# Optimization experiments

Hardware: AMD Instinct MI355X
Metric: run time of the kernel (lower is better)

Reference implementation:

```python
import jax, jax.numpy as jnp
import numpy as np
import math

H = 512      # d_model
N = 64       # d_state
B = 16
L = 4096
DT_MIN, DT_MAX = 0.001, 0.1


def setup_inputs() -> dict:
    key = jax.random.key(0)
    ks = jax.random.split(key, 6)
    u = jax.random.normal(ks[0], (B, H, L), dtype=jnp.float32)
    # S4DKernel parameters
    C = jax.random.normal(ks[1], (H, N // 2, 2), dtype=jnp.float32)  # view_as_real of cfloat C
    log_dt = (jax.random.uniform(ks[2], (H,), dtype=jnp.float32)
              * (math.log(DT_MAX) - math.log(DT_MIN)) + math.log(DT_MIN))
    log_A_real = jnp.log(0.5 * jnp.ones((H, N // 2), dtype=jnp.float32))
    A_imag = math.pi * jnp.broadcast_to(jnp.arange(N // 2, dtype=jnp.float32), (H, N // 2))
    # S4D parameters
    D = jax.random.normal(ks[3], (H,), dtype=jnp.float32)
    # output_linear: Conv1d(H, 2H, kernel_size=1) -> weight (2H, H), bias (2H,)
    W = jax.random.normal(ks[4], (2 * H, H), dtype=jnp.float32) * (1.0 / math.sqrt(H))
    b = jax.random.normal(ks[5], (2 * H,), dtype=jnp.float32) * 0.01
    return {"u": u, "C": C, "log_dt": log_dt, "log_A_real": log_A_real,
            "A_imag": A_imag, "D": D, "W": W, "b": b}


def _s4d_kernel(C, log_dt, log_A_real, A_imag, L):
    """Generate the (H, L) convolution kernel from diagonal SSM parameters."""
    dt = jnp.exp(log_dt)                                    # (H,)
    Cc = C[..., 0] + 1j * C[..., 1]                         # (H, N/2) complex
    A = -jnp.exp(log_A_real) + 1j * A_imag                  # (H, N/2)
    dtA = A * dt[:, None]                                   # (H, N/2)
    # Vandermonde: exp(dtA * l) for l in [0, L)
    K = jnp.exp(dtA[:, :, None] * jnp.arange(L, dtype=jnp.float32))  # (H, N/2, L)
    Cw = Cc * (jnp.exp(dtA) - 1.0) / A                      # (H, N/2)
    k = 2.0 * jnp.einsum('hn,hnl->hl', Cw, K).real          # (H, L)
    return k


def reference(u, C, log_dt, log_A_real, A_imag, D, W, b):
    Lc = u.shape[-1]
    k = _s4d_kernel(C, log_dt, log_A_real, A_imag, Lc)      # (H, L)
    # FFT long convolution (linear conv via zero-padding to 2L)
    k_f = jnp.fft.rfft(k, n=2 * Lc)                          # (H, L+1)
    u_f = jnp.fft.rfft(u, n=2 * Lc)                          # (B, H, L+1)
    y = jnp.fft.irfft(u_f * k_f, n=2 * Lc)[..., :Lc]         # (B, H, L)
    y = y + u * D[:, None]
    y = jax.nn.gelu(y, approximate=False)                    # torch nn.GELU default
    # output_linear: 1x1 Conv1d (H -> 2H) then GLU over channel dim
    z = jnp.einsum('oh,bhl->bol', W, y) + b[None, :, None]   # (B, 2H, L)
    a, g = jnp.split(z, 2, axis=1)
    return a * jax.nn.sigmoid(g)                             # (B, H, L)
```

## Files before the change

### kernel.cpp

```cpp
#include <hip/hip_runtime.h>

#define BB 16
#define HH 512
#define NH 32
#define LL 4096
#define TCH 64
#define NCH 64
#define KA 128

static_assert(TCH * NCH == LL, "chunking");

typedef __attribute__((ext_vector_type(8))) short bf16x8;
typedef __attribute__((ext_vector_type(4))) float f32x4;

static __device__ __forceinline__ unsigned short f2bf(float x) {
    return __builtin_bit_cast(unsigned short, (__bf16)x);
}
static __device__ __forceinline__ float bf2f(unsigned short b) {
    return __builtin_bit_cast(float, ((unsigned)b) << 16);
}
static __device__ __forceinline__ unsigned pack2(float a, float b) {
    return (unsigned)f2bf(a) | ((unsigned)f2bf(b) << 16);
}
static __device__ __forceinline__ float gelu1(float x) {
    float a = fmaf(0.071354816f * x, x * x, 1.5957691f * x);
    return x * __builtin_amdgcn_rcpf(1.0f + __expf(-a));
}
static __device__ __forceinline__ unsigned gelu_pk(unsigned p) {
    float a = gelu1(bf2f((unsigned short)(p & 0xffffu)));
    float b = gelu1(bf2f((unsigned short)(p >> 16)));
    return pack2(a, b);
}

static __device__ __forceinline__ void gload_lds16(const void* g, void* l) {
#if __has_builtin(__builtin_amdgcn_global_load_lds)
    __builtin_amdgcn_global_load_lds(
        (const __attribute__((address_space(1))) unsigned int*)g,
        (__attribute__((address_space(3))) unsigned int*)l, 16, 0, 0);
#else
    *(uint4*)l = *(const uint4*)g;
#endif
}

__global__ void k0_params(const float* __restrict__ C,
                          const float* __restrict__ log_dt,
                          const float* __restrict__ lAr,
                          const float* __restrict__ Aim,
                          float* __restrict__ c2R,  float* __restrict__ c2I,
                          float* __restrict__ ltR,  float* __restrict__ ltI,
                          float* __restrict__ xrA,  float* __restrict__ xiA)
{
    int tid = blockIdx.x * 256 + threadIdx.x;
    if (tid >= HH * NH) return;
    int h = tid >> 5;
    float dt = expf(log_dt[h]);
    float Ar = -expf(lAr[tid]);
    float Ai = Aim[tid];
    float xr = Ar * dt, xi = Ai * dt;
    xrA[tid] = xr; xiA[tid] = xi;
    float er = expf(xr);
    float lr = er * cosf(xi);
    float li = er * sinf(xi);
    float wr = lr - 1.0f, wi = li;
    float inv = 1.0f / (Ar * Ar + Ai * Ai);
    float qr = (wr * Ar + wi * Ai) * inv;
    float qi = (wi * Ar - wr * Ai) * inv;
    float cr = C[2 * tid], ci = C[2 * tid + 1];
    c2R[tid] =  2.0f * (cr * qr - ci * qi);
    c2I[tid] = -2.0f * (cr * qi + ci * qr);
    float eT = expf((float)TCH * xr);
    float aT = (float)TCH * xi;
    ltR[tid] = eT * cosf(aT);
    ltI[tid] = eT * sinf(aT);
}

__global__ void kw_pack(const float* __restrict__ W, const float* __restrict__ bias,
                        unsigned short* __restrict__ Wp, float* __restrict__ bp)
{
    int tid = blockIdx.x * 256 + threadIdx.x;
    int drow = tid >> 6;
    int kc = (tid & 63) * 8;
    int src = (drow & 1) ? (drow >> 1) + HH : (drow >> 1);
    const float4* s = (const float4*)(W + (size_t)src * HH + kc);
    float4 a = s[0], b4 = s[1];
    uint4 pack;
    pack.x = pack2(a.x, a.y);
    pack.y = pack2(a.z, a.w);
    pack.z = pack2(b4.x, b4.y);
    pack.w = pack2(b4.z, b4.w);
    *(uint4*)(Wp + (size_t)drow * HH + kc) = pack;
    if (tid < 2 * HH)
        bp[tid] = bias[(tid & 1) ? (tid >> 1) + HH : (tid >> 1)];
}

__global__ __launch_bounds__(64) void kA_build(
    const float* __restrict__ c2R, const float* __restrict__ c2I,
    const float* __restrict__ xrA, const float* __restrict__ xiA,
    const float* __restrict__ Dv,
    unsigned short* __restrict__ Apan, unsigned short* __restrict__ Vpan)
{
    int h = blockIdx.x;
    int t = threadIdx.x;
    __shared__ float s_xr[NH], s_xi[NH], s_cr[NH], s_ci[NH], s_k[TCH];
    if (t < NH) {
        s_xr[t] = xrA[h * NH + t]; s_xi[t] = xiA[h * NH + t];
        s_cr[t] = c2R[h * NH + t]; s_ci[t] = c2I[h * NH + t];
    }
    __syncthreads();
    {
        float d = (float)t;
        float acc = 0.f;
#pragma unroll
        for (int n = 0; n < NH; ++n) {
            float er = __expf(s_xr[n] * d);
            float sv, cv; __sincosf(s_xi[n] * d, &sv, &cv);
            acc = fmaf(s_cr[n], er * cv, fmaf(s_ci[n], er * sv, acc));
        }
        s_k[t] = acc;
    }
    __syncthreads();
    float k0d = s_k[0] + Dv[h];
    unsigned short row[KA];
#pragma unroll
    for (int tau = 0; tau < TCH; ++tau)
        row[tau] = f2bf((tau < t) ? s_k[t - tau] : (tau == t ? k0d : 0.f));
    float tp = (float)(t + 1);
#pragma unroll
    for (int n = 0; n < NH; ++n) {
        float er = __expf(s_xr[n] * tp);
        float sv, cv; __sincosf(s_xi[n] * tp, &sv, &cv);
        float pr = er * cv, pi = er * sv;
        row[TCH + 2 * n]     = f2bf(fmaf(s_cr[n], pr,  s_ci[n] * pi));
        row[TCH + 2 * n + 1] = f2bf(fmaf(s_ci[n], pr, -s_cr[n] * pi));
    }
    {
        uint4* dst = (uint4*)(Apan + ((size_t)h * TCH + t) * KA);
        const uint4* src = (const uint4*)row;
#pragma unroll
        for (int i = 0; i < 16; ++i) dst[i] = src[i];
    }
    {
        int n = t >> 1, cm = t & 1;
        float xr = s_xr[n], xi = s_xi[n];
        unsigned short vrow[TCH];
#pragma unroll
        for (int tau = 0; tau < TCH; ++tau) {
            float p = (float)(TCH - 1 - tau);
            float er = __expf(xr * p);
            float sv, cv; __sincosf(xi * p, &sv, &cv);
            vrow[tau] = f2bf(cm ? er * sv : er * cv);
        }
        uint4* vd = (uint4*)(Vpan + ((size_t)h * TCH + t) * TCH);
        const uint4* vs = (const uint4*)vrow;
#pragma unroll
        for (int i = 0; i < 8; ++i) vd[i] = vs[i];
    }
}

__global__ __launch_bounds__(256)
__attribute__((amdgpu_waves_per_eu(4, 4)))
void kBCD(
    const float* __restrict__ u,
    const unsigned short* __restrict__ Apan, const unsigned short* __restrict__ Vpan,
    const float* __restrict__ ltR, const float* __restrict__ ltI,
    unsigned short* __restrict__ yb)
{
    __shared__ unsigned short Sl[4][TCH * TCH];
    int h = blockIdx.x & (HH - 1), g = blockIdx.x >> 9;
    int tid = threadIdx.x;
    int lane = tid & 63, w = tid >> 6;
    int b = g * 4 + w;
    int lrow = lane & 15, hi = lane >> 4, lk8 = hi * 8;
    const float* ug = u + ((size_t)b * HH + h) * LL;
    const unsigned short* Ap = Apan + (size_t)h * TCH * KA;
    const unsigned short* Vp = Vpan + (size_t)h * TCH * TCH;
    char* Sw = (char*)Sl[w];

    bf16x8 ub[2][4];
#pragma unroll
    for (int ks = 0; ks < 2; ++ks)
#pragma unroll
        for (int n = 0; n < 4; ++n) {
            int c = n * 16 + lrow;
            const float* up = ug + c * TCH + ks * 32 + lk8;
            float4 f0 = *(const float4*)up, f1 = *(const float4*)(up + 4);
            bf16x8 v;
            v[0]=f2bf(f0.x); v[1]=f2bf(f0.y); v[2]=f2bf(f0.z); v[3]=f2bf(f0.w);
            v[4]=f2bf(f1.x); v[5]=f2bf(f1.y); v[6]=f2bf(f1.z); v[7]=f2bf(f1.w);
            ub[ks][n] = v;
        }

#pragma unroll
    for (int m = 0; m < 4; ++m) {
        f32x4 accE[4];
#pragma unroll
        for (int n = 0; n < 4; ++n) { f32x4 z = {0.f,0.f,0.f,0.f}; accE[n] = z; }
#pragma unroll
        for (int ks = 0; ks < 2; ++ks) {
            bf16x8 vf = *(const bf16x8*)(Vp + (m * 16 + lrow) * TCH + ks * 32 + lk8);
#pragma unroll
            for (int n = 0; n < 4; ++n)
                accE[n] = __builtin_amdgcn_mfma_f32_16x16x32_bf16(vf, ub[ks][n], accE[n], 0, 0, 0);
        }
        int j0 = m * 16 + hi * 4;
#pragma unroll
        for (int n = 0; n < 4; ++n) {
            int c = n * 16 + lrow;
            uint2 p; p.x = pack2(accE[n][0], accE[n][1]); p.y = pack2(accE[n][2], accE[n][3]);
            *(uint2*)(Sw + c * 128 + ((2 * j0) ^ ((c & 7) << 4))) = p;
        }
    }
    asm volatile("s_waitcnt lgkmcnt(0)" ::: "memory");

    if (lane < NH) {
        int n = lane;
        float ar = ltR[h * NH + n], ai = ltI[h * NH + n];
        float sr = 0.f, si = 0.f;
#pragma unroll
        for (int gg = 0; gg < 8; ++gg) {
            unsigned ev[8];
#pragma unroll
            for (int k = 0; k < 8; ++k)
                ev[k] = *(const unsigned*)(Sw + (gg * 8 + k) * 128 + ((4 * n) ^ (k << 4)));
#pragma unroll
            for (int k = 0; k < 8; ++k) {
                *(unsigned*)(Sw + (gg * 8 + k) * 128 + ((4 * n) ^ (k << 4))) = pack2(sr, si);
                float er = bf2f((unsigned short)(ev[k] & 0xffffu));
                float ei = bf2f((unsigned short)(ev[k] >> 16));
                float nsr = fmaf(ar, sr, fmaf(-ai, si, er));
                float nsi = fmaf(ar, si, fmaf(ai, sr, ei));
                sr = nsr; si = nsi;
            }
        }
    }
    asm volatile("s_waitcnt lgkmcnt(0)" ::: "memory");

    unsigned short* yrow = yb + ((size_t)b * HH + h) * LL;
#pragma unroll
    for (int m = 0; m < 4; ++m) {
        f32x4 acc[4];
#pragma unroll
        for (int n = 0; n < 4; ++n) { f32x4 z = {0.f,0.f,0.f,0.f}; acc[n] = z; }
#pragma unroll
        for (int ks = 0; ks < 2; ++ks) {
            bf16x8 af = *(const bf16x8*)(Ap + (m * 16 + lrow) * KA + ks * 32 + lk8);
#pragma unroll
            for (int n = 0; n < 4; ++n)
                acc[n] = __builtin_amdgcn_mfma_f32_16x16x32_bf16(af, ub[ks][n], acc[n], 0, 0, 0);
        }
#pragma unroll
        for (int ks = 0; ks < 2; ++ks) {
            bf16x8 af = *(const bf16x8*)(Ap + (m * 16 + lrow) * KA + 64 + ks * 32 + lk8);
#pragma unroll
            for (int n = 0; n < 4; ++n) {
                int c = n * 16 + lrow;
                bf16x8 bfr = *(const bf16x8*)(Sw + c * 128 + ((ks * 64 + lk8 * 2) ^ ((c & 7) << 4)));
                acc[n] = __builtin_amdgcn_mfma_f32_16x16x32_bf16(af, bfr, acc[n], 0, 0, 0);
            }
        }
        int t0 = m * 16 + hi * 4;
#pragma unroll
        for (int n = 0; n < 4; ++n) {
            int c = n * 16 + lrow;
            f32x4 v = acc[n];
            uint2 pw;
            pw.x = pack2(v[0], v[1]);
            pw.y = pack2(v[2], v[3]);
            *(uint2*)(yrow + c * TCH + t0) = pw;
        }
    }
}

__global__ __launch_bounds__(256) void kT_transpose(
    const unsigned short* __restrict__ yb, unsigned short* __restrict__ yt)
{
    __shared__ unsigned short T[64][130];
    int bid = blockIdx.x;
    int lt = bid & 31;
    int ht = (bid >> 5) & 7;
    int b  = bid >> 8;
    int t = threadIdx.x;
#pragma unroll
    for (int r = 0; r < 4; ++r) {
        int chunk = r * 256 + t;
        int row = chunk >> 4;
        int c16 = chunk & 15;
        uint4 v = *(const uint4*)(yb + ((size_t)(b * HH + ht * 64 + row)) * LL
                                     + lt * 128 + c16 * 8);
        v.x = gelu_pk(v.x); v.y = gelu_pk(v.y);
        v.z = gelu_pk(v.z); v.w = gelu_pk(v.w);
        *(uint4*)&T[row][c16 * 8] = v;
    }
    __syncthreads();
    int oct = t & 7, lgrp = t >> 3;
    size_t obase = ((size_t)b * LL + (size_t)lt * 128) * HH + ht * 64 + oct * 8;
#pragma unroll
    for (int r = 0; r < 2; ++r) {
        int l = (r * 32 + lgrp) * 2;
        unsigned v[8];
#pragma unroll
        for (int k = 0; k < 8; ++k)
            v[k] = *(const unsigned*)&T[oct * 8 + k][l];
        uint4 w0, w1;
        w0.x = (v[0] & 0xffffu) | (v[1] << 16);
        w0.y = (v[2] & 0xffffu) | (v[3] << 16);
        w0.z = (v[4] & 0xffffu) | (v[5] << 16);
        w0.w = (v[6] & 0xffffu) | (v[7] << 16);
        w1.x = (v[0] >> 16) | (v[1] & 0xffff0000u);
        w1.y = (v[2] >> 16) | (v[3] & 0xffff0000u);
        w1.z = (v[4] >> 16) | (v[5] & 0xffff0000u);
        w1.w = (v[6] >> 16) | (v[7] & 0xffff0000u);
        *(uint4*)(yt + obase + (size_t)l * HH) = w0;
        *(uint4*)(yt + obase + (size_t)(l + 1) * HH) = w1;
    }
}

#define BM 128
#define BN 128
#define BKK 32

__global__ __launch_bounds__(256, 4) void k4_gemm(
    const unsigned short* __restrict__ Wp, const float* __restrict__ bp,
    const unsigned short* __restrict__ yt, float* __restrict__ out)
{
    __shared__ unsigned short As[BM * BKK];
    __shared__ unsigned short Bs[BN * BKK];
    int tid  = threadIdx.x;
    int bidx = (blockIdx.x & 7) * 512 + (blockIdx.x >> 3);
    int mtile = bidx & 7, ntile = bidx >> 3;
    int mbase = mtile * BM, nbase = ntile * BN;
    int lane = tid & 63;
    int wv = tid >> 6;
    int wr = wv >> 1, wc = wv & 1;
    int lrow = lane & 15;
    int hi = lane >> 4;

    f32x4 acc[4][4];
#pragma unroll
    for (int m = 0; m < 4; ++m)
#pragma unroll
        for (int n = 0; n < 4; ++n) { f32x4 z = {0.f,0.f,0.f,0.f}; acc[m][n] = z; }

    for (int kk = 0; kk < HH; kk += BKK) {
#pragma unroll
        for (int p = 0; p < 2; ++p) {
            int chunk = p * 256 + tid;
            int row = chunk >> 2;
            int c16 = chunk & 3;
            int kc  = (c16 ^ ((row >> 1) & 3)) * 8;
            gload_lds16(Wp + (size_t)(mbase + row) * HH + kk + kc, &As[chunk * 8]);
            gload_lds16(yt + (size_t)(nbase + row) * HH + kk + kc, &Bs[chunk * 8]);
        }
        __syncthreads();
        bf16x8 af[4], bfr[4];
#pragma unroll
        for (int m = 0; m < 4; ++m) {
            int row = wr * 64 + m * 16 + lrow;
            int slot = hi ^ ((row >> 1) & 3);
            af[m] = *(const bf16x8*)&As[row * BKK + slot * 8];
        }
#pragma unroll
        for (int nf = 0; nf < 4; ++nf) {
            int row = wc * 64 + nf * 16 + lrow;
            int slot = hi ^ ((row >> 1) & 3);
            bfr[nf] = *(const bf16x8*)&Bs[row * BKK + slot * 8];
        }
#pragma unroll
        for (int m = 0; m < 4; ++m)
#pragma unroll
            for (int nf = 0; nf < 4; ++nf)
                acc[m][nf] = __builtin_amdgcn_mfma_f32_16x16x32_bf16(af[m], bfr[nf], acc[m][nf], 0, 0, 0);
        __syncthreads();
    }
#pragma unroll
    for (int m = 0; m < 4; ++m) {
        int go = mbase + wr * 64 + m * 16 + (hi * 4);
        float4 bv = *(const float4*)(bp + go);
#pragma unroll
        for (int nf = 0; nf < 4; ++nf) {
            int col  = nbase + wc * 64 + nf * 16 + lrow;
            int bcol = col >> 12;
            int lcol = col & (LL - 1);
            f32x4 v = acc[m][nf];
            float a0 = v[0] + bv.x, g0 = v[1] + bv.y;
            float a1 = v[2] + bv.z, g1 = v[3] + bv.w;
            float o0 = a0 / (1.0f + __expf(-g0));
            float o1 = a1 / (1.0f + __expf(-g1));
            size_t ob = ((size_t)bcol * HH + (size_t)(go >> 1)) * LL + lcol;
            out[ob] = o0;
            out[ob + LL] = o1;
        }
    }
}

extern "C" void kernel_launch(void* const* d_in, const int* in_sizes, int n_in,
                              void* d_out, int out_size, void* d_ws, size_t ws_size,
                              hipStream_t stream) {
    const float* u    = (const float*)d_in[0];
    const float* C    = (const float*)d_in[1];
    const float* ldt  = (const float*)d_in[2];
    const float* lar  = (const float*)d_in[3];
    const float* aim  = (const float*)d_in[4];
    const float* Dv   = (const float*)d_in[5];
    const float* W    = (const float*)d_in[6];
    const float* bias = (const float*)d_in[7];
    float* out = (float*)d_out;

    char* w = (char*)d_ws;
    float* c2R = (float*)w; w += (size_t)HH * NH * 4;
    float* c2I = (float*)w; w += (size_t)HH * NH * 4;
    float* ltR = (float*)w; w += (size_t)HH * NH * 4;
    float* ltI = (float*)w; w += (size_t)HH * NH * 4;
    float* xrA = (float*)w; w += (size_t)HH * NH * 4;
    float* xiA = (float*)w; w += (size_t)HH * NH * 4;
    float* bp  = (float*)w; w += (size_t)2 * HH * 4;
    unsigned short* Wp   = (unsigned short*)w; w += (size_t)2 * HH * HH * 2;
    unsigned short* Apan = (unsigned short*)w; w += (size_t)HH * TCH * KA * 2;
    unsigned short* Vpan = (unsigned short*)w; w += (size_t)HH * TCH * TCH * 2;
    unsigned short* yt   = (unsigned short*)w; w += (size_t)BB * LL * HH * 2;

    unsigned short* yb = (unsigned short*)d_out;

    k0_params   <<<dim3(64),   dim3(256), 0, stream>>>(C, ldt, lar, aim, c2R, c2I, ltR, ltI, xrA, xiA);
    kw_pack     <<<dim3(256),  dim3(256), 0, stream>>>(W, bias, Wp, bp);
    kA_build    <<<dim3(512),  dim3(64),  0, stream>>>(c2R, c2I, xrA, xiA, Dv, Apan, Vpan);
    kBCD        <<<dim3(2048), dim3(256), 0, stream>>>(u, Apan, Vpan, ltR, ltI, yb);
    kT_transpose<<<dim3(4096), dim3(256), 0, stream>>>(yb, yt);
    k4_gemm     <<<dim3(4096), dim3(256), 0, stream>>>(Wp, bp, yt, out);
}
```

Before: 195.6 us.

## Stage kBCD output through LDS for coalesced 16-byte stores, hoist state fragments

The S-state MFMA operand fragments are loaded from LDS once into registers instead of being reloaded for every m-tile. The packed bf16 results are held in registers, written into the per-wave swizzled LDS tile, then copied to global memory as contiguous 16-byte stores instead of scattered 8-byte stores. The occupancy hint is relaxed from exactly 4 waves per EU to a minimum of 2, giving the compiler room for the extra registers at the cost of possible lower occupancy.

```diff
diff --git a/kernel.cpp b/kernel.cpp
--- a/kernel.cpp
+++ b/kernel.cpp
@@ -158,7 +158,7 @@
 }
 
 __global__ __launch_bounds__(256)
-__attribute__((amdgpu_waves_per_eu(4, 4)))
+__attribute__((amdgpu_waves_per_eu(2)))
 void kBCD(
     const float* __restrict__ u,
     const unsigned short* __restrict__ Apan, const unsigned short* __restrict__ Vpan,
@@ -235,7 +235,16 @@
     }
     asm volatile("s_waitcnt lgkmcnt(0)" ::: "memory");
 
-    unsigned short* yrow = yb + ((size_t)b * HH + h) * LL;
+    bf16x8 sfr[2][4];
+#pragma unroll
+    for (int ks = 0; ks < 2; ++ks)
+#pragma unroll
+        for (int n = 0; n < 4; ++n) {
+            int c = n * 16 + lrow;
+            sfr[ks][n] = *(const bf16x8*)(Sw + c * 128 + ((ks * 64 + lk8 * 2) ^ ((c & 7) << 4)));
+        }
+
+    uint2 yp[4][4];
 #pragma unroll
     for (int m = 0; m < 4; ++m) {
         f32x4 acc[4];
@@ -252,22 +261,35 @@
         for (int ks = 0; ks < 2; ++ks) {
             bf16x8 af = *(const bf16x8*)(Ap + (m * 16 + lrow) * KA + 64 + ks * 32 + lk8);
 #pragma unroll
-            for (int n = 0; n < 4; ++n) {
-                int c = n * 16 + lrow;
-                bf16x8 bfr = *(const bf16x8*)(Sw + c * 128 + ((ks * 64 + lk8 * 2) ^ ((c & 7) << 4)));
-                acc[n] = __builtin_amdgcn_mfma_f32_16x16x32_bf16(af, bfr, acc[n], 0, 0, 0);
-            }
-        }
-        int t0 = m * 16 + hi * 4;
+            for (int n = 0; n < 4; ++n)
+                acc[n] = __builtin_amdgcn_mfma_f32_16x16x32_bf16(af, sfr[ks][n], acc[n], 0, 0, 0);
+        }
+#pragma unroll
+        for (int n = 0; n < 4; ++n) {
+            yp[m][n].x = pack2(acc[n][0], acc[n][1]);
+            yp[m][n].y = pack2(acc[n][2], acc[n][3]);
+        }
+    }
+    asm volatile("s_waitcnt lgkmcnt(0)" ::: "memory");
+
+#pragma unroll
+    for (int m = 0; m < 4; ++m) {
+        int t0b = m * 32 + hi * 8;
 #pragma unroll
         for (int n = 0; n < 4; ++n) {
             int c = n * 16 + lrow;
-            f32x4 v = acc[n];
-            uint2 pw;
-            pw.x = pack2(v[0], v[1]);
-            pw.y = pack2(v[2], v[3]);
-            *(uint2*)(yrow + c * TCH + t0) = pw;
-        }
+            *(uint2*)(Sw + c * 128 + (t0b ^ ((c & 7) << 4))) = yp[m][n];
+        }
+    }
+    asm volatile("s_waitcnt lgkmcnt(0)" ::: "memory");
+    unsigned short* yrow = yb + ((size_t)b * HH + h) * LL;
+#pragma unroll
+    for (int it = 0; it < 8; ++it) {
+        int o = it * 1024 + lane * 16;
+        int c = o >> 7;
+        int sl = o & 127;
+        uint4 v = *(const uint4*)(Sw + c * 128 + (sl ^ ((c & 7) << 4)));
+        *(uint4*)((char*)yrow + o) = v;
     }
 }
 
```

New measurement: 184.0 us. 1.06x faster.
